# Optimization experiments

Hardware: AMD Instinct MI355X
Metric: run time of the kernel (lower is better)

## Reference

```python
import jax, jax.numpy as jnp
import numpy as np

# Module hyperparameters (must satisfy R == T*T for the torch .view to be valid)
NUM_NODE_TYPES = 2   # T
NUM_REL_TYPES = 4    # R
NUM_BASES = 8
N_NODES = 100_000
N_EDGES = 1_600_000
IN_DIM = 64
OUT_DIM = 64
M = NUM_REL_TYPES * NUM_NODE_TYPES * NUM_NODE_TYPES  # 16 distinct relation matrices


def setup_inputs() -> dict:
    key = jax.random.key(0)
    ks = jax.random.split(key, 8)
    x = jax.random.normal(ks[0], (N_NODES, IN_DIM), dtype=jnp.float32)
    node_type = jax.random.randint(ks[1], (N_NODES,), 0, NUM_NODE_TYPES, dtype=jnp.int32)
    edge_src = jax.random.randint(ks[2], (N_EDGES,), 0, N_NODES, dtype=jnp.int32)
    edge_dst = jax.random.randint(ks[3], (N_EDGES,), 0, N_NODES, dtype=jnp.int32)
    edge_type = jax.random.randint(ks[4], (N_EDGES,), 0, NUM_REL_TYPES, dtype=jnp.int32)
    # learned params (xavier-ish scales)
    weight = jax.random.normal(ks[5], (NUM_BASES, IN_DIM, OUT_DIM), dtype=jnp.float32) * 0.05
    w_comp = jax.random.normal(ks[6], (M, NUM_BASES), dtype=jnp.float32) * 0.3
    bias = jax.random.normal(ks[7], (1, OUT_DIM), dtype=jnp.float32) * 0.1
    return {"x": x, "node_type": node_type, "edge_src": edge_src, "edge_dst": edge_dst,
            "edge_type": edge_type, "weight": weight, "w_comp": w_comp, "bias": bias}


def reference(x, node_type, edge_src, edge_dst, edge_type, weight, w_comp, bias):
    T, R = NUM_NODE_TYPES, NUM_REL_TYPES
    n_nodes = x.shape[0]
    # Faithful to torch: weight.view(out, B, in); matmul broadcasts (M,B) x (out,B,in) -> (out,M,in);
    # then .view(R*R, out, in) is a raw memory reinterpretation (valid because M == R*R).
    w_flat = weight.reshape(OUT_DIM, NUM_BASES, IN_DIM)
    comb = jnp.matmul(w_comp, w_flat)               # (out, M, in)
    W = comb.reshape(M, OUT_DIM, IN_DIM)            # (M, out, in)
    # Per-edge relation index: src_type*T*R + dst_type*R + edge_type
    rel = node_type[edge_src] * (T * R) + node_type[edge_dst] * R + edge_type  # (E,)
    # msg_e = W[rel_e] @ x[src_e]. Since there are only M=16 distinct matrices,
    # transform every node by every matrix once (N*M*out), then gather per edge;
    # same math, avoids materializing an (E,out,in) gather. Dropout is run in
    # eval mode (identity) for a deterministic reference.
    all_msgs = jnp.einsum('ni,moi->nmo', x, W)      # (N, M, out)
    msg = all_msgs[edge_src, rel]                   # (E, out)
    agg = jax.ops.segment_sum(msg, edge_dst, num_segments=n_nodes)  # (N, out)
    out = agg + bias                                # add_bias=True; activation=None
    return out
```

## Files before the change

### kernel.cpp

```cpp
#include <hip/hip_runtime.h>
#include <stdint.h>


#define TPB 256
#define DPB 32

#define A8IDX(ld, c) (((ld) * 8 + (c)) * 76 + (((ld) & 6) << 1))

__global__ void k_build_w(const float* __restrict__ weight,
                          const float* __restrict__ w_comp,
                          float* __restrict__ Wt) {
  const int idx = blockIdx.x * TPB + threadIdx.x;
  if (idx >= 16 * 64 * 64) return;
  const int m = idx >> 12, i = (idx >> 6) & 63, o = idx & 63;
  const float* wc = w_comp + ((o & 15) << 3);
  const float* wf = weight + (((m << 2) + (o >> 4)) << 9) + i;
  float s = 0.f;
#pragma unroll
  for (int b = 0; b < 8; ++b) s = fmaf(wc[b], wf[b << 6], s);
  Wt[idx] = s;
}

__global__ void k_zero(int* __restrict__ p, int n) {
  const int i = blockIdx.x * 1024 + threadIdx.x;
  if (i < n) p[i] = 0;
}

__global__ void k_hist(const int* __restrict__ edst, int* __restrict__ cntD, int E) {
  const int e = blockIdx.x * TPB + threadIdx.x;
  if (e < E) atomicAdd(&cntD[edst[e]], 1);
}

#define SCAN_T 1024
__global__ void k_scan(const int* __restrict__ cnt, int* __restrict__ offs,
                       int* __restrict__ cursor, int N) {
  __shared__ int ps[SCAN_T];
  const int tid = threadIdx.x;
  const int chunk = (N + SCAN_T - 1) / SCAN_T;
  const int b = tid * chunk, e = min(b + chunk, N);
  int s = 0;
  for (int i = b; i < e; ++i) s += cnt[i];
  ps[tid] = s;
  __syncthreads();
  for (int off = 1; off < SCAN_T; off <<= 1) {
    int v = 0;
    if (tid >= off) v = ps[tid - off];
    __syncthreads();
    ps[tid] += v;
    __syncthreads();
  }
  int run = (tid > 0) ? ps[tid - 1] : 0;
  for (int i = b; i < e; ++i) { offs[i] = run; cursor[i] = run; run += cnt[i]; }
  if (tid == SCAN_T - 1) offs[N] = run;
}

__global__ void k_scatter(const int* __restrict__ nt, const int* __restrict__ esrc,
                          const int* __restrict__ edst, const int* __restrict__ etyp,
                          int* __restrict__ cursor, uint32_t* __restrict__ packS, int E) {
  const int e = blockIdx.x * TPB + threadIdx.x;
  if (e < E) {
    const int s = esrc[e];
    const uint32_t r8 = (uint32_t)(nt[s] * 4 + etyp[e]);
    const int pos = atomicAdd(&cursor[edst[e]], 1);
    packS[pos] = (uint32_t)s | (r8 << 24);
  }
}

__global__ __launch_bounds__(TPB) void k_main(
    const float* __restrict__ x, const float* __restrict__ Wt,
    const int* __restrict__ offsD, const uint32_t* __restrict__ packS,
    const int* __restrict__ nt, const float* __restrict__ bias,
    float* __restrict__ out, int N) {
  __shared__ float A8[DPB * 8 * 76 + 16];
  __shared__ int offs[DPB + 1];
  __shared__ int ntl[DPB];
  const int tid = threadIdx.x;
  const int d0 = blockIdx.x * DPB;
  const int nd = min(DPB, N - d0);
  if (tid <= nd) offs[tid] = offsD[d0 + tid];
  if (tid < nd) ntl[tid] = nt[d0 + tid];
  __syncthreads();

  const int w = tid >> 6, lane = tid & 63;
  for (int ld = w; ld < DPB; ld += 4) {
    float racc[8] = {0.f, 0.f, 0.f, 0.f, 0.f, 0.f, 0.f, 0.f};
    if (ld < nd) {
      const int j0 = offs[ld], j1 = offs[ld + 1];
      for (int j = j0; j < j1; j += 8) {
        uint32_t pk[8];
        float xv[8];
#pragma unroll
        for (int u = 0; u < 8; ++u) {
          const int jj = min(j + u, j1 - 1);
          pk[u] = packS[jj];
        }
#pragma unroll
        for (int u = 0; u < 8; ++u)
          xv[u] = x[((size_t)(pk[u] & 0x00FFFFFFu) << 6) + lane];
#pragma unroll
        for (int u = 0; u < 8; ++u) {
          const float v = (j + u < j1) ? xv[u] : 0.f;
          switch (pk[u] >> 24) {
            case 0: racc[0] += v; break;
            case 1: racc[1] += v; break;
            case 2: racc[2] += v; break;
            case 3: racc[3] += v; break;
            case 4: racc[4] += v; break;
            case 5: racc[5] += v; break;
            case 6: racc[6] += v; break;
            default: racc[7] += v; break;
          }
        }
      }
    }
#pragma unroll
    for (int c = 0; c < 8; ++c) A8[A8IDX(ld, c) + lane] = racc[c];
  }
  __syncthreads();

  const int co = tid & 15, re = tid >> 4;
  const int ld0 = re * 2, ld1 = re * 2 + 1;
  float acc[2][4];
#pragma unroll
  for (int j = 0; j < 4; ++j) {
    const float bv = bias[(co << 2) + j];
    acc[0][j] = bv;
    acc[1][j] = bv;
  }
  const int t0 = (ld0 < nd) ? ntl[ld0] : 0;
  const int t1 = (ld1 < nd) ? ntl[ld1] : 0;
  const float4* Wt4 = (const float4*)Wt;
#pragma unroll 2
  for (int r8 = 0; r8 < 8; ++r8) {
    const int rel0 = ((r8 >> 2) << 3) + (t0 << 2) + (r8 & 3);
    const int rel1 = ((r8 >> 2) << 3) + (t1 << 2) + (r8 & 3);
    const float4* wp0 = Wt4 + (rel0 << 10) + co;
    const float4* wp1 = Wt4 + (rel1 << 10) + co;
    const float* a0 = &A8[A8IDX(ld0, r8)];
    const float* a1 = &A8[A8IDX(ld1, r8)];
    for (int k4 = 0; k4 < 64; k4 += 4) {
      const float4 av0 = *(const float4*)(a0 + k4);
      const float4 av1 = *(const float4*)(a1 + k4);
#pragma unroll
      for (int kk = 0; kk < 4; ++kk) {
        const float4 w0 = wp0[(k4 + kk) << 4];
        const float4 w1 = wp1[(k4 + kk) << 4];
        const float f0 = ((const float*)&av0)[kk];
        const float f1 = ((const float*)&av1)[kk];
        acc[0][0] = fmaf(f0, w0.x, acc[0][0]); acc[0][1] = fmaf(f0, w0.y, acc[0][1]);
        acc[0][2] = fmaf(f0, w0.z, acc[0][2]); acc[0][3] = fmaf(f0, w0.w, acc[0][3]);
        acc[1][0] = fmaf(f1, w1.x, acc[1][0]); acc[1][1] = fmaf(f1, w1.y, acc[1][1]);
        acc[1][2] = fmaf(f1, w1.z, acc[1][2]); acc[1][3] = fmaf(f1, w1.w, acc[1][3]);
      }
    }
  }

  if (ld0 < nd) {
    float4 v = {acc[0][0], acc[0][1], acc[0][2], acc[0][3]};
    *(float4*)(out + ((size_t)(d0 + ld0) << 6) + (co << 2)) = v;
  }
  if (ld1 < nd) {
    float4 v = {acc[1][0], acc[1][1], acc[1][2], acc[1][3]};
    *(float4*)(out + ((size_t)(d0 + ld1) << 6) + (co << 2)) = v;
  }
}

extern "C" void kernel_launch(void* const* d_in, const int* in_sizes, int n_in,
                              void* d_out, int out_size, void* d_ws, size_t ws_size,
                              hipStream_t stream) {
  const float* x      = (const float*)d_in[0];
  const int* nt       = (const int*)d_in[1];
  const int* esrc     = (const int*)d_in[2];
  const int* edst     = (const int*)d_in[3];
  const int* etyp     = (const int*)d_in[4];
  const float* weight = (const float*)d_in[5];
  const float* w_comp = (const float*)d_in[6];
  const float* bias   = (const float*)d_in[7];
  float* out = (float*)d_out;
  const int N = in_sizes[1];
  const int E = in_sizes[2];

  char* wsp = (char*)d_ws;
  size_t off = 0;
  float* Wt = (float*)(wsp + off); off += 262144;
  int* cntD = (int*)(wsp + off); off += (size_t)N * 4;
  int* offsD = (int*)(wsp + off); off += (size_t)(N + 1) * 4 + 12;
  int* cursor = (int*)(wsp + off); off += (size_t)N * 4;
  uint32_t* packS = (uint32_t*)(wsp + off); off += (size_t)E * 4;
  if (ws_size < off) return;

  const int ebl = (E + TPB - 1) / TPB;

  hipLaunchKernelGGL(k_zero, dim3((N + 1023) / 1024), dim3(1024), 0, stream, cntD, N);
  hipLaunchKernelGGL(k_build_w, dim3(256), dim3(TPB), 0, stream, weight, w_comp, Wt);
  hipLaunchKernelGGL(k_hist, dim3(ebl), dim3(TPB), 0, stream, edst, cntD, E);
  hipLaunchKernelGGL(k_scan, dim3(1), dim3(SCAN_T), 0, stream, cntD, offsD, cursor, N);
  hipLaunchKernelGGL(k_scatter, dim3(ebl), dim3(TPB), 0, stream, nt, esrc, edst, etyp,
                     cursor, packS, E);
  hipLaunchKernelGGL(k_main, dim3((N + DPB - 1) / DPB), dim3(TPB), 0, stream,
                     x, Wt, offsD, packS, nt, bias, out, N);
}
```

Baseline: 1.758 ms.

## Group destination nodes by type and stage relation weights in shared memory

Adds a node-type histogram and scatter that permute destination nodes so every block handles nodes of a single type. Because all nodes in a block then share the same 8 relation matrices, each 64x64 matrix is staged into LDS once per relation and reused by all 16 destinations, replacing per-thread global float4 weight loads. DPB is halved to 16 and launch bounds request 3 blocks per CU. The cost is two extra small kernels, more __syncthreads per block, and scattered output writes through the permutation.

```diff
diff --git a/kernel.cpp b/kernel.cpp
--- a/kernel.cpp
+++ b/kernel.cpp
@@ -3,9 +3,8 @@
 
 
 #define TPB 256
-#define DPB 32
-
-#define A8IDX(ld, c) (((ld) * 8 + (c)) * 76 + (((ld) & 6) << 1))
+#define DPB 16
+#define ASTR (8*64 + 4)
 
 __global__ void k_build_w(const float* __restrict__ weight,
                           const float* __restrict__ w_comp,
@@ -31,9 +30,15 @@
   if (e < E) atomicAdd(&cntD[edst[e]], 1);
 }
 
+__global__ void k_typehist(const int* __restrict__ nt, int* __restrict__ typeCnt, int N) {
+  const int i = blockIdx.x * TPB + threadIdx.x;
+  if (i < N) atomicAdd(&typeCnt[nt[i]], 1);
+}
+
 #define SCAN_T 1024
 __global__ void k_scan(const int* __restrict__ cnt, int* __restrict__ offs,
-                       int* __restrict__ cursor, int N) {
+                       int* __restrict__ cursor, const int* __restrict__ typeCnt,
+                       int* __restrict__ tblk, int N) {
   __shared__ int ps[SCAN_T];
   const int tid = threadIdx.x;
   const int chunk = (N + SCAN_T - 1) / SCAN_T;
@@ -52,6 +57,16 @@
   int run = (tid > 0) ? ps[tid - 1] : 0;
   for (int i = b; i < e; ++i) { offs[i] = run; cursor[i] = run; run += cnt[i]; }
   if (tid == SCAN_T - 1) offs[N] = run;
+  if (tid == 0) { tblk[0] = typeCnt[0]; tblk[1] = 0; tblk[2] = typeCnt[0]; }
+}
+
+__global__ void k_typescatter(const int* __restrict__ nt, int* __restrict__ tcur,
+                              int* __restrict__ dstPerm, int N) {
+  const int i = blockIdx.x * TPB + threadIdx.x;
+  if (i < N) {
+    const int pos = atomicAdd(&tcur[nt[i]], 1);
+    dstPerm[pos] = i;
+  }
 }
 
 __global__ void k_scatter(const int* __restrict__ nt, const int* __restrict__ esrc,
@@ -66,26 +81,42 @@
   }
 }
 
-__global__ __launch_bounds__(TPB) void k_main(
+__global__ __launch_bounds__(TPB, 3) void k_main(
     const float* __restrict__ x, const float* __restrict__ Wt,
     const int* __restrict__ offsD, const uint32_t* __restrict__ packS,
-    const int* __restrict__ nt, const float* __restrict__ bias,
-    float* __restrict__ out, int N) {
-  __shared__ float A8[DPB * 8 * 76 + 16];
-  __shared__ int offs[DPB + 1];
-  __shared__ int ntl[DPB];
+    const int* __restrict__ dstPerm, const int* __restrict__ tblk,
+    const float* __restrict__ bias, float* __restrict__ out, int N) {
+  __shared__ float A8[DPB * ASTR];
+  __shared__ float Wl[64 * 64];
+  __shared__ int dstl[DPB], offA[DPB], offB[DPB];
+  __shared__ int shn0;
   const int tid = threadIdx.x;
-  const int d0 = blockIdx.x * DPB;
-  const int nd = min(DPB, N - d0);
-  if (tid <= nd) offs[tid] = offsD[d0 + tid];
-  if (tid < nd) ntl[tid] = nt[d0 + tid];
+  if (tid == 0) shn0 = tblk[0];
+  __syncthreads();
+  const int n0 = shn0;
+  const int nb0 = (n0 + DPB - 1) / DPB;
+  const int nb1 = (N - n0 + DPB - 1) / DPB;
+  int t, base, cnt;
+  if ((int)blockIdx.x < nb0) {
+    t = 0; base = blockIdx.x * DPB; cnt = min(DPB, n0 - base);
+  } else if ((int)blockIdx.x < nb0 + nb1) {
+    t = 1; base = n0 + (blockIdx.x - nb0) * DPB; cnt = min(DPB, N - base);
+  } else {
+    return;
+  }
+  if (tid < cnt) {
+    const int d = dstPerm[base + tid];
+    dstl[tid] = d;
+    offA[tid] = offsD[d];
+    offB[tid] = offsD[d + 1];
+  }
   __syncthreads();
 
   const int w = tid >> 6, lane = tid & 63;
   for (int ld = w; ld < DPB; ld += 4) {
     float racc[8] = {0.f, 0.f, 0.f, 0.f, 0.f, 0.f, 0.f, 0.f};
-    if (ld < nd) {
-      const int j0 = offs[ld], j1 = offs[ld + 1];
+    if (ld < cnt) {
+      const int j0 = offA[ld], j1 = offB[ld];
       for (int j = j0; j < j1; j += 8) {
         uint32_t pk[8];
         float xv[8];
@@ -114,54 +145,39 @@
       }
     }
 #pragma unroll
-    for (int c = 0; c < 8; ++c) A8[A8IDX(ld, c) + lane] = racc[c];
-  }
-  __syncthreads();
+    for (int c = 0; c < 8; ++c) A8[ld * ASTR + c * 64 + lane] = racc[c];
+  }
 
   const int co = tid & 15, re = tid >> 4;
-  const int ld0 = re * 2, ld1 = re * 2 + 1;
-  float acc[2][4];
-#pragma unroll
-  for (int j = 0; j < 4; ++j) {
-    const float bv = bias[(co << 2) + j];
-    acc[0][j] = bv;
-    acc[1][j] = bv;
-  }
-  const int t0 = (ld0 < nd) ? ntl[ld0] : 0;
-  const int t1 = (ld1 < nd) ? ntl[ld1] : 0;
-  const float4* Wt4 = (const float4*)Wt;
-#pragma unroll 2
+  const float4 bv = ((const float4*)bias)[co];
+  float a0 = bv.x, a1 = bv.y, a2 = bv.z, a3 = bv.w;
+#pragma unroll 1
   for (int r8 = 0; r8 < 8; ++r8) {
-    const int rel0 = ((r8 >> 2) << 3) + (t0 << 2) + (r8 & 3);
-    const int rel1 = ((r8 >> 2) << 3) + (t1 << 2) + (r8 & 3);
-    const float4* wp0 = Wt4 + (rel0 << 10) + co;
-    const float4* wp1 = Wt4 + (rel1 << 10) + co;
-    const float* a0 = &A8[A8IDX(ld0, r8)];
-    const float* a1 = &A8[A8IDX(ld1, r8)];
+    const int rel = ((r8 >> 2) << 3) + (t << 2) + (r8 & 3);
+    __syncthreads();
+    {
+      const float4* src = (const float4*)(Wt + (rel << 12));
+      float4* dst4 = (float4*)Wl;
+#pragma unroll
+      for (int u = 0; u < 4; ++u) dst4[tid + (u << 8)] = src[tid + (u << 8)];
+    }
+    __syncthreads();
+    const float* arow = &A8[re * ASTR + (r8 << 6)];
+#pragma unroll 4
     for (int k4 = 0; k4 < 64; k4 += 4) {
-      const float4 av0 = *(const float4*)(a0 + k4);
-      const float4 av1 = *(const float4*)(a1 + k4);
+      const float4 av = *(const float4*)(arow + k4);
 #pragma unroll
       for (int kk = 0; kk < 4; ++kk) {
-        const float4 w0 = wp0[(k4 + kk) << 4];
-        const float4 w1 = wp1[(k4 + kk) << 4];
-        const float f0 = ((const float*)&av0)[kk];
-        const float f1 = ((const float*)&av1)[kk];
-        acc[0][0] = fmaf(f0, w0.x, acc[0][0]); acc[0][1] = fmaf(f0, w0.y, acc[0][1]);
-        acc[0][2] = fmaf(f0, w0.z, acc[0][2]); acc[0][3] = fmaf(f0, w0.w, acc[0][3]);
-        acc[1][0] = fmaf(f1, w1.x, acc[1][0]); acc[1][1] = fmaf(f1, w1.y, acc[1][1]);
-        acc[1][2] = fmaf(f1, w1.z, acc[1][2]); acc[1][3] = fmaf(f1, w1.w, acc[1][3]);
+        const float4 wv = *(const float4*)&Wl[((k4 + kk) << 6) + (co << 2)];
+        const float f = ((const float*)&av)[kk];
+        a0 = fmaf(f, wv.x, a0); a1 = fmaf(f, wv.y, a1);
+        a2 = fmaf(f, wv.z, a2); a3 = fmaf(f, wv.w, a3);
       }
     }
   }
-
-  if (ld0 < nd) {
-    float4 v = {acc[0][0], acc[0][1], acc[0][2], acc[0][3]};
-    *(float4*)(out + ((size_t)(d0 + ld0) << 6) + (co << 2)) = v;
-  }
-  if (ld1 < nd) {
-    float4 v = {acc[1][0], acc[1][1], acc[1][2], acc[1][3]};
-    *(float4*)(out + ((size_t)(d0 + ld1) << 6) + (co << 2)) = v;
+  if (re < cnt) {
+    float4 v = {a0, a1, a2, a3};
+    *(float4*)(out + ((size_t)dstl[re] << 6) + (co << 2)) = v;
   }
 }
 
@@ -182,21 +198,29 @@
 
   char* wsp = (char*)d_ws;
   size_t off = 0;
-  float* Wt = (float*)(wsp + off); off += 262144;
-  int* cntD = (int*)(wsp + off); off += (size_t)N * 4;
-  int* offsD = (int*)(wsp + off); off += (size_t)(N + 1) * 4 + 12;
-  int* cursor = (int*)(wsp + off); off += (size_t)N * 4;
+  float* Wt       = (float*)(wsp + off); off += 262144;
+  int* cntD       = (int*)(wsp + off); off += (size_t)(N + 2) * 4 + 8;
+  int* offsD      = (int*)(wsp + off); off += (size_t)(N + 1) * 4 + 12;
+  int* cursor     = (int*)(wsp + off); off += (size_t)N * 4;
+  int* tblk       = (int*)(wsp + off); off += 16;
+  int* dstPerm    = (int*)(wsp + off); off += (size_t)N * 4;
   uint32_t* packS = (uint32_t*)(wsp + off); off += (size_t)E * 4;
   if (ws_size < off) return;
+  int* typeCnt = cntD + N;
 
   const int ebl = (E + TPB - 1) / TPB;
-
-  hipLaunchKernelGGL(k_zero, dim3((N + 1023) / 1024), dim3(1024), 0, stream, cntD, N);
+  const int nbl = (N + TPB - 1) / TPB;
+
+  hipLaunchKernelGGL(k_zero, dim3((N + 2 + 1023) / 1024), dim3(1024), 0, stream, cntD, N + 2);
   hipLaunchKernelGGL(k_build_w, dim3(256), dim3(TPB), 0, stream, weight, w_comp, Wt);
   hipLaunchKernelGGL(k_hist, dim3(ebl), dim3(TPB), 0, stream, edst, cntD, E);
-  hipLaunchKernelGGL(k_scan, dim3(1), dim3(SCAN_T), 0, stream, cntD, offsD, cursor, N);
+  hipLaunchKernelGGL(k_typehist, dim3(nbl), dim3(TPB), 0, stream, nt, typeCnt, N);
+  hipLaunchKernelGGL(k_scan, dim3(1), dim3(SCAN_T), 0, stream, cntD, offsD, cursor,
+                     typeCnt, tblk, N);
+  hipLaunchKernelGGL(k_typescatter, dim3(nbl), dim3(TPB), 0, stream, nt, tblk + 1,
+                     dstPerm, N);
   hipLaunchKernelGGL(k_scatter, dim3(ebl), dim3(TPB), 0, stream, nt, esrc, edst, etyp,
                      cursor, packS, E);
-  hipLaunchKernelGGL(k_main, dim3((N + DPB - 1) / DPB), dim3(TPB), 0, stream,
-                     x, Wt, offsD, packS, nt, bias, out, N);
-}
+  hipLaunchKernelGGL(k_main, dim3(N / DPB + 2), dim3(TPB), 0, stream,
+                     x, Wt, offsD, packS, dstPerm, tblk, bias, out, N);
+}
```

New measurement: 2.284 ms. 29.9% more time.
